# Performance work log

Measured on AMD Instinct MI355X. Metric: run time of the kernel, lower is better.

The kernel has to match this reference:

```python
import jax, jax.numpy as jnp
import numpy as np

EPS = 1e-06  # SCORE_SCALE_EPSILON
SCORE_MARGIN = 0.0
SCORE_SCALE = 1.0


def setup_inputs() -> dict:
    key = jax.random.key(0)
    k1, k2, k3, k4, k5 = jax.random.split(key, 5)
    B, N, d = 1024, 40000, 512
    # scale 0.05 keeps points well inside the Poincare ball for c <= 0.01
    query = jax.random.normal(k1, (B, d), dtype=jnp.float32) * 0.05
    candidates = jax.random.normal(k2, (N, d), dtype=jnp.float32) * 0.05
    candidate_bias = jax.random.normal(k3, (N,), dtype=jnp.float32) * 0.01
    # per-query local curvature in (0.001, 0.01)
    query_curvature = jax.random.uniform(k4, (B,), dtype=jnp.float32) * 0.009 + 0.001
    target = jax.random.randint(k5, (B,), 0, N)
    return {"query": query, "candidates": candidates,
            "candidate_bias": candidate_bias,
            "query_curvature": query_curvature, "target": target}


def _hyperbolic_ce(query, candidates, candidate_bias, query_curvature, target):
    # query: [B,d], candidates: [N,d], c_q: [B,1]
    c_q = query_curvature[:, None]
    sqrt_c = jnp.sqrt(c_q + EPS)                                  # [B,1]
    x_sq = jnp.sum(query * query, axis=-1, keepdims=True)        # [B,1]
    y_sq = jnp.sum(candidates * candidates, axis=-1)[None, :]    # [1,N]
    xy = jnp.einsum('bd,nd->bn', query, candidates)              # [B,N] Gram (GEMM)
    # mobius_add(-x, y, c) = (A*(-x) + Bc*y) / denom, with per-pair scalars:
    A = 1.0 - 2.0 * c_q * xy + c_q * y_sq                        # [B,N]
    Bc = 1.0 - c_q * x_sq                                        # [B,1]
    # ||A*(-x) + Bc*y||^2 expanded algebraically (avoids [B,N,d] tensor)
    num_sq = A * A * x_sq - 2.0 * A * Bc * xy + Bc * Bc * y_sq
    denom = 1.0 - 2.0 * c_q * xy + (c_q * c_q) * x_sq * y_sq
    diff_norm = jnp.sqrt(jnp.maximum(num_sq, 0.0)) / (denom + EPS)
    diff_norm = jnp.maximum(diff_norm, EPS)                      # clamp(min=EPS)
    max_norm = 1.0 / (sqrt_c + EPS) - EPS
    diff_norm = jnp.minimum(diff_norm, max_norm)
    dist = (2.0 / (sqrt_c + EPS)) * jnp.arctanh(
        jnp.minimum(sqrt_c * diff_norm, 1.0 - EPS))
    logits = SCORE_SCALE * (SCORE_MARGIN - dist) + candidate_bias[None, :]
    lse = jax.scipy.special.logsumexp(logits, axis=1)            # [B]
    tgt_logits = jnp.take_along_axis(logits, target[:, None], axis=1)[:, 0]
    return jnp.mean(lse - tgt_logits)


def reference(query, candidates, candidate_bias, query_curvature, target):
    return _hyperbolic_ce(query, candidates, candidate_bias, query_curvature, target)
```

## Files before the change

kernel.cpp:

```cpp
#include <hip/hip_runtime.h>
#include <math.h>

#define EPSF 1e-6f
#define NB    1024
#define ND    512
#define NCAND 40000
#define NPAD  40064
#define NCHUNK 626
#define LOG2E 1.44269504088896340736f

typedef __attribute__((ext_vector_type(8))) short          bf16x8;
typedef __attribute__((ext_vector_type(8))) unsigned short ushort8;
typedef __attribute__((ext_vector_type(4))) float          f32x4;

__device__ __forceinline__ unsigned short f2bf(float f) {
  union { float f; unsigned int u; } v; v.f = f;
  unsigned int u = v.u;
  return (unsigned short)((u + 0x7FFFu + ((u >> 16) & 1u)) >> 16);
}

__device__ __forceinline__ void gload_lds16(const void* g, void* l) {
  __builtin_amdgcn_global_load_lds(
      (const __attribute__((address_space(1))) void*)g,
      (__attribute__((address_space(3))) void*)l, 16, 0, 0);
}

__global__ __launch_bounds__(256) void prep_all_kernel(
    const float* __restrict__ q, const float* __restrict__ cand,
    const float* __restrict__ bias, const float* __restrict__ curv,
    const int* __restrict__ target,
    unsigned short* __restrict__ qb, unsigned short* __restrict__ cb,
    float* __restrict__ ysq, float4* __restrict__ rcst,
    float* __restrict__ b2, float* __restrict__ tgtl)
{
  const int blk = blockIdx.x;
  const int tid = threadIdx.x, wid = tid >> 6, lane = tid & 63;

  {
    const long row = (long)blk * 4 + wid;
    float vals[8];
    if (row < NCAND) {
      const float4* s = (const float4*)(cand + row * ND + lane * 8);
      float4 a = s[0], b = s[1];
      vals[0]=a.x; vals[1]=a.y; vals[2]=a.z; vals[3]=a.w;
      vals[4]=b.x; vals[5]=b.y; vals[6]=b.z; vals[7]=b.w;
    } else {
      #pragma unroll
      for (int i = 0; i < 8; ++i) vals[i] = 0.f;
    }
    float ss = 0.f; ushort8 o;
    #pragma unroll
    for (int i = 0; i < 8; ++i) { ss = fmaf(vals[i], vals[i], ss); o[i] = f2bf(vals[i]); }
    *(ushort8*)(cb + row * ND + lane * 8) = o;
    #pragma unroll
    for (int m = 1; m < 64; m <<= 1) ss += __shfl_xor(ss, m, 64);
    if (lane == 0) ysq[row] = ss;
  }

  if (blk >= 256) return;

  {
    const int g = blk * 256 + tid;
    if (g < NPAD) b2[g] = (g < NCAND) ? bias[g] * LOG2E : -INFINITY;
  }

  {
    const long row = (long)blk * 4 + wid;
    const float4* s = (const float4*)(q + row * ND + lane * 8);
    float4 a = s[0], b = s[1];
    float vals[8] = {a.x,a.y,a.z,a.w,b.x,b.y,b.z,b.w};
    float ss = 0.f; ushort8 o;
    #pragma unroll
    for (int i = 0; i < 8; ++i) { ss = fmaf(vals[i], vals[i], ss); o[i] = f2bf(vals[i]); }
    *(ushort8*)(qb + row * ND + lane * 8) = o;
    #pragma unroll
    for (int m = 1; m < 64; m <<= 1) ss += __shfl_xor(ss, m, 64);
    if (lane == 0) {
      const float c   = curv[row];
      const float scv = sqrtf(c + EPSF);
      const float inv = 1.f / (scv + EPSF);
      rcst[row] = make_float4(-c, fmaf(-c, ss, 1.f), inv, 2.f * c * c * ss);
    }
  }

  {
    const int b = blk * 4 + wid;
    const int t = target[b];
    const float4* qp = (const float4*)(q + (long)b * ND + lane * 8);
    const float4* cp = (const float4*)(cand + (long)t * ND + lane * 8);
    float4 a0 = qp[0], a1 = qp[1], c0 = cp[0], c1 = cp[1];
    float qa[8] = {a0.x,a0.y,a0.z,a0.w,a1.x,a1.y,a1.z,a1.w};
    float ca[8] = {c0.x,c0.y,c0.z,c0.w,c1.x,c1.y,c1.z,c1.w};
    float xy = 0.f, xs = 0.f, ys = 0.f;
    #pragma unroll
    for (int i = 0; i < 8; ++i) {
      xy = fmaf(qa[i], ca[i], xy);
      xs = fmaf(qa[i], qa[i], xs);
      ys = fmaf(ca[i], ca[i], ys);
    }
    #pragma unroll
    for (int m = 1; m < 64; m <<= 1) {
      xy += __shfl_xor(xy, m, 64);
      xs += __shfl_xor(xs, m, 64);
      ys += __shfl_xor(ys, m, 64);
    }
    if (lane == 0) {
      float c  = curv[b];
      float sc = sqrtf(c + EPSF);
      float A  = 1.f - 2.f * c * xy + c * ys;
      float Bc = 1.f - c * xs;
      float nsq = A * A * xs - 2.f * A * Bc * xy + Bc * Bc * ys;
      float den = 1.f - 2.f * c * xy + c * c * xs * ys;
      float dn  = sqrtf(fmaxf(nsq, 0.f)) / (den + EPSF);
      dn = fminf(fmaxf(dn, EPSF), 1.f / (sc + EPSF) - EPSF);
      float tt  = fminf(sc * dn, 1.f - EPSF);
      float dist = 2.f / (sc + EPSF) * atanhf(tt);
      tgtl[b] = bias[t] - dist;
    }
  }
}

__global__ __launch_bounds__(256, 4) void gemm_epi_kernel(
    const unsigned short* __restrict__ Qb,
    const unsigned short* __restrict__ Cb,
    const float4* __restrict__ rcst,
    const float* __restrict__ ysq,
    const float* __restrict__ b2,
    float* __restrict__ partials)
{
  __shared__ unsigned short As[128 * 64];
  __shared__ unsigned short Bs[128 * 64];
  const int tid  = threadIdx.x;
  const int lane = tid & 63;
  const int wid  = tid >> 6;
  const int wr   = wid >> 1, wc = wid & 1;
  const int l15  = lane & 15, l4 = lane >> 4;

  const int h  = blockIdx.x;
  const int w  = (h & 7) * 313 + (h >> 3);
  const int bm = w & 7, bn = w >> 3;

  f32x4 acc[4][4] = {};

  const unsigned short* qbase = Qb + (long)bm * 128 * ND;
  const unsigned short* cbase = Cb + (long)bn * 128 * ND;

  for (int k0 = 0; k0 < ND; k0 += 64) {
    __syncthreads();
    #pragma unroll
    for (int j = 0; j < 4; ++j) {
      const int e = j * 256 + tid;
      const int r = e >> 3;
      const int c = ((e & 7) ^ (r & 7)) * 8;
      gload_lds16(qbase + (long)r * ND + k0 + c, &As[e * 8]);
      gload_lds16(cbase + (long)r * ND + k0 + c, &Bs[e * 8]);
    }
    __syncthreads();
    #pragma unroll
    for (int kk = 0; kk < 2; ++kk) {
      bf16x8 a[4], b[4];
      const int kb = (kk * 32 + l4 * 8) * 2;
      #pragma unroll
      for (int i = 0; i < 4; ++i) {
        const int row = wr * 64 + i * 16 + l15;
        a[i] = *(const bf16x8*)((const char*)As + row * 128 + (kb ^ ((row & 7) << 4)));
      }
      #pragma unroll
      for (int j = 0; j < 4; ++j) {
        const int row = wc * 64 + j * 16 + l15;
        b[j] = *(const bf16x8*)((const char*)Bs + row * 128 + (kb ^ ((row & 7) << 4)));
      }
      #pragma unroll
      for (int i = 0; i < 4; ++i)
        #pragma unroll
        for (int j = 0; j < 4; ++j)
          acc[i][j] = __builtin_amdgcn_mfma_f32_16x16x32_bf16(a[i], b[j], acc[i][j], 0, 0, 0);
    }
  }

  const int rbase = bm * 128 + wr * 64;
  const int cb0   = bn * 128 + wc * 64 + l15;
  float ysv[4], bv[4];
  #pragma unroll
  for (int j = 0; j < 4; ++j) { ysv[j] = ysq[cb0 + j * 16]; bv[j] = b2[cb0 + j * 16]; }

  #pragma unroll
  for (int i = 0; i < 4; ++i) {
    #pragma unroll
    for (int r = 0; r < 4; ++r) {
      const int grow = rbase + i * 16 + l4 * 4 + r;
      const float4 rc = rcst[grow];
      const float negc = rc.x, Bc = rc.y, inv = rc.z, c2xs2 = rc.w;
      const float n4c = 4.f * negc;
      float s = 0.f;
      #pragma unroll
      for (int j = 0; j < 4; ++j) {
        const float xy   = acc[i][j][r];
        const float By   = fmaf(negc, ysv[j], 1.f);
        const float P    = Bc * By;
        const float den2 = fmaf(c2xs2, ysv[j], fmaf(n4c, xy, 2.f));
        const float wv   = fmaf(den2, __builtin_amdgcn_rcpf(P), -1.f);
        const float t2   = fmaxf(fmaf(wv, wv, -1.f), 0.f);
        const float W    = wv + __builtin_amdgcn_sqrtf(t2);
        const float lg   = __builtin_amdgcn_logf(W);
        s += __builtin_amdgcn_exp2f(fmaf(-inv, lg, bv[j]));
      }
      s += __shfl_xor(s, 1, 64);
      s += __shfl_xor(s, 2, 64);
      s += __shfl_xor(s, 4, 64);
      s += __shfl_xor(s, 8, 64);
      if (l15 == 0) partials[(long)grow * NCHUNK + (bn * 2 + wc)] = s;
    }
  }
}

__global__ __launch_bounds__(128) void lse_row_kernel(
    const float* __restrict__ partials, const float* __restrict__ tgtl,
    float* __restrict__ rowloss)
{
  const int b = blockIdx.x;
  const int tid = threadIdx.x;
  float s = 0.f;
  for (int i = tid; i < NCHUNK; i += 128) s += partials[(long)b * NCHUNK + i];
  #pragma unroll
  for (int m = 1; m < 64; m <<= 1) s += __shfl_xor(s, m, 64);
  __shared__ float red[2];
  if ((tid & 63) == 0) red[tid >> 6] = s;
  __syncthreads();
  if (tid == 0) rowloss[b] = logf(red[0] + red[1]) - tgtl[b];
}

__global__ __launch_bounds__(256) void final_sum_kernel(
    const float* __restrict__ rowloss, float* __restrict__ out)
{
  const int tid = threadIdx.x;
  float s = rowloss[tid] + rowloss[tid + 256] + rowloss[tid + 512] + rowloss[tid + 768];
  #pragma unroll
  for (int m = 1; m < 64; m <<= 1) s += __shfl_xor(s, m, 64);
  __shared__ float red[4];
  if ((tid & 63) == 0) red[tid >> 6] = s;
  __syncthreads();
  if (tid == 0) out[0] = (red[0] + red[1] + red[2] + red[3]) * (1.0f / (float)NB);
}

extern "C" void kernel_launch(void* const* d_in, const int* in_sizes, int n_in,
                              void* d_out, int out_size, void* d_ws, size_t ws_size,
                              hipStream_t stream) {
  const float* q    = (const float*)d_in[0];
  const float* cand = (const float*)d_in[1];
  const float* bias = (const float*)d_in[2];
  const float* curv = (const float*)d_in[3];
  const int*   tgt  = (const int*)d_in[4];
  float* out = (float*)d_out;

  char* ws = (char*)d_ws;
  unsigned short* cb = (unsigned short*)(ws);
  unsigned short* qb = (unsigned short*)(ws + 41025536);
  float*  ysq        = (float*) (ws + 42074112);
  float*  b2         = (float*) (ws + 42234368);
  float4* rcst       = (float4*)(ws + 42394624);
  float*  tgtl       = (float*) (ws + 42411008);
  float*  rowloss    = (float*) (ws + 42415104);
  float*  partials   = (float*) (ws + 42419200);

  prep_all_kernel<<<NPAD / 4, 256, 0, stream>>>(q, cand, bias, curv, tgt,
                                                qb, cb, ysq, rcst, b2, tgtl);
  gemm_epi_kernel<<<2504, 256, 0, stream>>>(qb, cb, rcst, ysq, b2, partials);
  lse_row_kernel<<<NB, 128, 0, stream>>>(partials, tgtl, rowloss);
  final_sum_kernel<<<1, 256, 0, stream>>>(rowloss, out);
}
```

Baseline: 191.0 us.

## Double-buffer LDS tiles with BK=32 to overlap global loads and MFMA

Splits the shared-memory tiles into two 32-wide K buffers and prefetches the next K slice with direct global-to-LDS loads while MFMAs run on the current one. LDS offsets are precomputed outside the loop and the swizzle is adapted to 64-byte rows. MFMA sections are wrapped in s_setprio to raise wave priority during compute. The aim is to hide global load latency behind compute, at the cost of twice as many barrier steps.

After: 200.5 us. 5.0% more time.

```diff
diff --git a/kernel.cpp b/kernel.cpp
--- a/kernel.cpp
+++ b/kernel.cpp
@@ -128,8 +128,8 @@
     const float* __restrict__ b2,
     float* __restrict__ partials)
 {
-  __shared__ unsigned short As[128 * 64];
-  __shared__ unsigned short Bs[128 * 64];
+  __shared__ unsigned short As[2][128 * 32];
+  __shared__ unsigned short Bs[2][128 * 32];
   const int tid  = threadIdx.x;
   const int lane = tid & 63;
   const int wid  = tid >> 6;
@@ -145,38 +145,61 @@
   const unsigned short* qbase = Qb + (long)bm * 128 * ND;
   const unsigned short* cbase = Cb + (long)bn * 128 * ND;
 
-  for (int k0 = 0; k0 < ND; k0 += 64) {
+  const int e0 = tid, e1 = 256 + tid;
+  const int r0 = e0 >> 2, r1 = e1 >> 2;
+  const int g0 = ((e0 & 3) ^ (r0 & 3)) * 8;
+  const int g1 = ((e1 & 3) ^ (r1 & 3)) * 8;
+  const unsigned short* qs0 = qbase + (long)r0 * ND + g0;
+  const unsigned short* qs1 = qbase + (long)r1 * ND + g1;
+  const unsigned short* cs0 = cbase + (long)r0 * ND + g0;
+  const unsigned short* cs1 = cbase + (long)r1 * ND + g1;
+  const int d0 = e0 * 8, d1 = e1 * 8;
+
+  int aoff[4], boff[4];
+  #pragma unroll
+  for (int i = 0; i < 4; ++i) {
+    const int ra = wr * 64 + i * 16 + l15;
+    const int rb = wc * 64 + i * 16 + l15;
+    const int sw = (l4 * 16) ^ ((l15 & 3) << 4);
+    aoff[i] = ra * 64 + sw;
+    boff[i] = rb * 64 + sw;
+  }
+
+#define STAGE(B, KOF) do { \
+    gload_lds16(qs0 + (KOF), &As[B][d0]); \
+    gload_lds16(qs1 + (KOF), &As[B][d1]); \
+    gload_lds16(cs0 + (KOF), &Bs[B][d0]); \
+    gload_lds16(cs1 + (KOF), &Bs[B][d1]); \
+  } while (0)
+
+#define COMPUTE(B) do { \
+    bf16x8 a[4], b[4]; \
+    _Pragma("unroll") \
+    for (int i = 0; i < 4; ++i) a[i] = *(const bf16x8*)((const char*)As[B] + aoff[i]); \
+    _Pragma("unroll") \
+    for (int j = 0; j < 4; ++j) b[j] = *(const bf16x8*)((const char*)Bs[B] + boff[j]); \
+    __builtin_amdgcn_s_setprio(1); \
+    _Pragma("unroll") \
+    for (int i = 0; i < 4; ++i) \
+      _Pragma("unroll") \
+      for (int j = 0; j < 4; ++j) \
+        acc[i][j] = __builtin_amdgcn_mfma_f32_16x16x32_bf16(a[i], b[j], acc[i][j], 0, 0, 0); \
+    __builtin_amdgcn_s_setprio(0); \
+  } while (0)
+
+  STAGE(0, 0);
+  __syncthreads();
+  #pragma unroll 1
+  for (int t = 0; t < 16; t += 2) {
+    STAGE(1, (t + 1) * 32);
+    COMPUTE(0);
     __syncthreads();
-    #pragma unroll
-    for (int j = 0; j < 4; ++j) {
-      const int e = j * 256 + tid;
-      const int r = e >> 3;
-      const int c = ((e & 7) ^ (r & 7)) * 8;
-      gload_lds16(qbase + (long)r * ND + k0 + c, &As[e * 8]);
-      gload_lds16(cbase + (long)r * ND + k0 + c, &Bs[e * 8]);
-    }
+    if (t < 14) STAGE(0, (t + 2) * 32);
+    COMPUTE(1);
     __syncthreads();
-    #pragma unroll
-    for (int kk = 0; kk < 2; ++kk) {
-      bf16x8 a[4], b[4];
-      const int kb = (kk * 32 + l4 * 8) * 2;
-      #pragma unroll
-      for (int i = 0; i < 4; ++i) {
-        const int row = wr * 64 + i * 16 + l15;
-        a[i] = *(const bf16x8*)((const char*)As + row * 128 + (kb ^ ((row & 7) << 4)));
-      }
-      #pragma unroll
-      for (int j = 0; j < 4; ++j) {
-        const int row = wc * 64 + j * 16 + l15;
-        b[j] = *(const bf16x8*)((const char*)Bs + row * 128 + (kb ^ ((row & 7) << 4)));
-      }
-      #pragma unroll
-      for (int i = 0; i < 4; ++i)
-        #pragma unroll
-        for (int j = 0; j < 4; ++j)
-          acc[i][j] = __builtin_amdgcn_mfma_f32_16x16x32_bf16(a[i], b[j], acc[i][j], 0, 0, 0);
-    }
-  }
+  }
+#undef STAGE
+#undef COMPUTE
 
   const int rbase = bm * 128 + wr * 64;
   const int cb0   = bn * 128 + wc * 64 + l15;
```

## Enlarge GEMM tiles to 256x256 with double-buffered LDS and in-block partial reduction

Applied to the files above, without the earlier changes.

The fused GEMM+epilogue kernel moves from 128x128 tiles with 256 threads to 256x256 tiles with 512 threads and 8 waves, each wave holding an 8x4 MFMA accumulator grid. Global-to-LDS loads are double-buffered so the next K slice loads while the current one computes, and MFMA sections are raised with s_setprio. Per-wave row partial sums are combined in LDS before a single store per row, shrinking the partials array and the row-LSE kernel's work. The costs are more LDS and registers per block and fewer blocks (628) over the CUs, plus padding N to 40192.

After: 236.5 us. +23.8%, slower.

```diff
diff --git a/kernel.cpp b/kernel.cpp
--- a/kernel.cpp
+++ b/kernel.cpp
@@ -5,8 +5,8 @@
 #define NB    1024
 #define ND    512
 #define NCAND 40000
-#define NPAD  40064
-#define NCHUNK 626
+#define NPAD  40192
+#define NCHUNK 157
 #define LOG2E 1.44269504088896340736f
 
 typedef __attribute__((ext_vector_type(8))) short          bf16x8;
@@ -120,7 +120,7 @@
   }
 }
 
-__global__ __launch_bounds__(256, 4) void gemm_epi_kernel(
+__global__ __launch_bounds__(512, 2) void gemm_epi_kernel(
     const unsigned short* __restrict__ Qb,
     const unsigned short* __restrict__ Cb,
     const float4* __restrict__ rcst,
@@ -128,106 +128,143 @@
     const float* __restrict__ b2,
     float* __restrict__ partials)
 {
-  __shared__ unsigned short As[128 * 64];
-  __shared__ unsigned short Bs[128 * 64];
+  __shared__ unsigned short As[2][256 * 64];
+  __shared__ unsigned short Bs[2][256 * 64];
+
   const int tid  = threadIdx.x;
   const int lane = tid & 63;
   const int wid  = tid >> 6;
-  const int wr   = wid >> 1, wc = wid & 1;
+  const int wr   = wid >> 2;
+  const int wc   = wid & 3;
   const int l15  = lane & 15, l4 = lane >> 4;
 
-  const int h  = blockIdx.x;
-  const int w  = (h & 7) * 313 + (h >> 3);
-  const int bm = w & 7, bn = w >> 3;
-
-  f32x4 acc[4][4] = {};
-
-  const unsigned short* qbase = Qb + (long)bm * 128 * ND;
-  const unsigned short* cbase = Cb + (long)bn * 128 * ND;
-
-  for (int k0 = 0; k0 < ND; k0 += 64) {
+  const int orig = blockIdx.x;
+  const int xcd  = orig & 7;
+  const int base = (xcd < 4) ? xcd * 79 : 316 + (xcd - 4) * 78;
+  const int wg   = base + (orig >> 3);
+  const int bm   = wg & 3, bn = wg >> 2;
+
+  f32x4 acc[8][4] = {};
+
+  const unsigned short* qbase = Qb + (long)bm * 256 * ND;
+  const unsigned short* cbase = Cb + (long)bn * 256 * ND;
+
+  const unsigned short* qsrc[4];
+  const unsigned short* csrc[4];
+  #pragma unroll
+  for (int j = 0; j < 4; ++j) {
+    const int e = j * 512 + tid;
+    const int r = e >> 3;
+    const int s = ((e & 7) ^ (r & 7)) * 8;
+    qsrc[j] = qbase + (long)r * ND + s;
+    csrc[j] = cbase + (long)r * ND + s;
+  }
+
+  int moff[8], noff[4];
+  #pragma unroll
+  for (int m = 0; m < 8; ++m) {
+    const int row = wr * 128 + m * 16 + l15;
+    moff[m] = row * 128 + ((l4 << 4) ^ ((row & 7) << 4));
+  }
+  #pragma unroll
+  for (int n = 0; n < 4; ++n) {
+    const int row = wc * 64 + n * 16 + l15;
+    noff[n] = row * 128 + ((l4 << 4) ^ ((row & 7) << 4));
+  }
+
+#define STAGE8(BUF, T) do { \
+    const long ko = (long)(T) * 64; \
+    _Pragma("unroll") \
+    for (int j = 0; j < 4; ++j) { \
+      const int d = (j * 512 + tid) * 8; \
+      gload_lds16(qsrc[j] + ko, &As[BUF][d]); \
+      gload_lds16(csrc[j] + ko, &Bs[BUF][d]); \
+    } \
+  } while (0)
+
+  STAGE8(0, 0);
+  __syncthreads();
+
+  #pragma unroll 2
+  for (int t = 0; t < 8; ++t) {
+    const int p = t & 1;
+    if (t < 7) STAGE8(p ^ 1, t + 1);
+    #pragma unroll
+    for (int kk = 0; kk < 2; ++kk) {
+      const int kx = kk << 6;
+      bf16x8 a[8], b[4];
+      #pragma unroll
+      for (int m = 0; m < 8; ++m)
+        a[m] = *(const bf16x8*)((const char*)As[p] + (moff[m] ^ kx));
+      #pragma unroll
+      for (int n = 0; n < 4; ++n)
+        b[n] = *(const bf16x8*)((const char*)Bs[p] + (noff[n] ^ kx));
+      __builtin_amdgcn_s_setprio(1);
+      #pragma unroll
+      for (int m = 0; m < 8; ++m)
+        #pragma unroll
+        for (int n = 0; n < 4; ++n)
+          acc[m][n] = __builtin_amdgcn_mfma_f32_16x16x32_bf16(a[m], b[n], acc[m][n], 0, 0, 0);
+      __builtin_amdgcn_s_setprio(0);
+    }
     __syncthreads();
-    #pragma unroll
-    for (int j = 0; j < 4; ++j) {
-      const int e = j * 256 + tid;
-      const int r = e >> 3;
-      const int c = ((e & 7) ^ (r & 7)) * 8;
-      gload_lds16(qbase + (long)r * ND + k0 + c, &As[e * 8]);
-      gload_lds16(cbase + (long)r * ND + k0 + c, &Bs[e * 8]);
-    }
-    __syncthreads();
-    #pragma unroll
-    for (int kk = 0; kk < 2; ++kk) {
-      bf16x8 a[4], b[4];
-      const int kb = (kk * 32 + l4 * 8) * 2;
-      #pragma unroll
-      for (int i = 0; i < 4; ++i) {
-        const int row = wr * 64 + i * 16 + l15;
-        a[i] = *(const bf16x8*)((const char*)As + row * 128 + (kb ^ ((row & 7) << 4)));
-      }
-      #pragma unroll
-      for (int j = 0; j < 4; ++j) {
-        const int row = wc * 64 + j * 16 + l15;
-        b[j] = *(const bf16x8*)((const char*)Bs + row * 128 + (kb ^ ((row & 7) << 4)));
-      }
-      #pragma unroll
-      for (int i = 0; i < 4; ++i)
-        #pragma unroll
-        for (int j = 0; j < 4; ++j)
-          acc[i][j] = __builtin_amdgcn_mfma_f32_16x16x32_bf16(a[i], b[j], acc[i][j], 0, 0, 0);
-    }
-  }
-
-  const int rbase = bm * 128 + wr * 64;
-  const int cb0   = bn * 128 + wc * 64 + l15;
+  }
+#undef STAGE8
+
+  float* scr = (float*)&As[0][0];
+  const int cb0 = bn * 256 + wc * 64 + l15;
   float ysv[4], bv[4];
   #pragma unroll
-  for (int j = 0; j < 4; ++j) { ysv[j] = ysq[cb0 + j * 16]; bv[j] = b2[cb0 + j * 16]; }
-
-  #pragma unroll
-  for (int i = 0; i < 4; ++i) {
+  for (int n = 0; n < 4; ++n) { ysv[n] = ysq[cb0 + n * 16]; bv[n] = b2[cb0 + n * 16]; }
+
+  #pragma unroll
+  for (int m = 0; m < 8; ++m) {
     #pragma unroll
     for (int r = 0; r < 4; ++r) {
-      const int grow = rbase + i * 16 + l4 * 4 + r;
+      const int lrow = wr * 128 + m * 16 + l4 * 4 + r;
+      const int grow = bm * 256 + lrow;
       const float4 rc = rcst[grow];
       const float negc = rc.x, Bc = rc.y, inv = rc.z, c2xs2 = rc.w;
       const float n4c = 4.f * negc;
       float s = 0.f;
       #pragma unroll
-      for (int j = 0; j < 4; ++j) {
-        const float xy   = acc[i][j][r];
-        const float By   = fmaf(negc, ysv[j], 1.f);
+      for (int n = 0; n < 4; ++n) {
+        const float xy   = acc[m][n][r];
+        const float By   = fmaf(negc, ysv[n], 1.f);
         const float P    = Bc * By;
-        const float den2 = fmaf(c2xs2, ysv[j], fmaf(n4c, xy, 2.f));
+        const float den2 = fmaf(c2xs2, ysv[n], fmaf(n4c, xy, 2.f));
         const float wv   = fmaf(den2, __builtin_amdgcn_rcpf(P), -1.f);
         const float t2   = fmaxf(fmaf(wv, wv, -1.f), 0.f);
         const float W    = wv + __builtin_amdgcn_sqrtf(t2);
         const float lg   = __builtin_amdgcn_logf(W);
-        s += __builtin_amdgcn_exp2f(fmaf(-inv, lg, bv[j]));
+        s += __builtin_amdgcn_exp2f(fmaf(-inv, lg, bv[n]));
       }
       s += __shfl_xor(s, 1, 64);
       s += __shfl_xor(s, 2, 64);
       s += __shfl_xor(s, 4, 64);
       s += __shfl_xor(s, 8, 64);
-      if (l15 == 0) partials[(long)grow * NCHUNK + (bn * 2 + wc)] = s;
-    }
-  }
-}
-
-__global__ __launch_bounds__(128) void lse_row_kernel(
+      if (l15 == 0) scr[lrow * 4 + wc] = s;
+    }
+  }
+  __syncthreads();
+  if (tid < 256) {
+    const float v = scr[tid * 4 + 0] + scr[tid * 4 + 1]
+                  + scr[tid * 4 + 2] + scr[tid * 4 + 3];
+    partials[(long)(bm * 256 + tid) * NCHUNK + bn] = v;
+  }
+}
+
+__global__ __launch_bounds__(64) void lse_row_kernel(
     const float* __restrict__ partials, const float* __restrict__ tgtl,
     float* __restrict__ rowloss)
 {
   const int b = blockIdx.x;
   const int tid = threadIdx.x;
   float s = 0.f;
-  for (int i = tid; i < NCHUNK; i += 128) s += partials[(long)b * NCHUNK + i];
+  for (int i = tid; i < NCHUNK; i += 64) s += partials[(long)b * NCHUNK + i];
   #pragma unroll
   for (int m = 1; m < 64; m <<= 1) s += __shfl_xor(s, m, 64);
-  __shared__ float red[2];
-  if ((tid & 63) == 0) red[tid >> 6] = s;
-  __syncthreads();
-  if (tid == 0) rowloss[b] = logf(red[0] + red[1]) - tgtl[b];
+  if (tid == 0) rowloss[b] = logf(s) - tgtl[b];
 }
 
 __global__ __launch_bounds__(256) void final_sum_kernel(
@@ -255,17 +292,17 @@
 
   char* ws = (char*)d_ws;
   unsigned short* cb = (unsigned short*)(ws);
-  unsigned short* qb = (unsigned short*)(ws + 41025536);
-  float*  ysq        = (float*) (ws + 42074112);
-  float*  b2         = (float*) (ws + 42234368);
-  float4* rcst       = (float4*)(ws + 42394624);
-  float*  tgtl       = (float*) (ws + 42411008);
-  float*  rowloss    = (float*) (ws + 42415104);
-  float*  partials   = (float*) (ws + 42419200);
+  unsigned short* qb = (unsigned short*)(ws + 41156608);
+  float*  ysq        = (float*) (ws + 42205184);
+  float*  b2         = (float*) (ws + 42365952);
+  float4* rcst       = (float4*)(ws + 42526720);
+  float*  tgtl       = (float*) (ws + 42543104);
+  float*  rowloss    = (float*) (ws + 42547200);
+  float*  partials   = (float*) (ws + 42551296);
 
   prep_all_kernel<<<NPAD / 4, 256, 0, stream>>>(q, cand, bias, curv, tgt,
                                                 qb, cb, ysq, rcst, b2, tgtl);
-  gemm_epi_kernel<<<2504, 256, 0, stream>>>(qb, cb, rcst, ysq, b2, partials);
-  lse_row_kernel<<<NB, 128, 0, stream>>>(partials, tgtl, rowloss);
+  gemm_epi_kernel<<<628, 512, 0, stream>>>(qb, cb, rcst, ysq, b2, partials);
+  lse_row_kernel<<<NB, 64, 0, stream>>>(partials, tgtl, rowloss);
   final_sum_kernel<<<1, 256, 0, stream>>>(rowloss, out);
 }
```
